# Optimization experiments

Hardware: AMD Instinct MI355X
Metric: run time of the kernel (lower is better)

The kernel has to match this reference:

```python
import jax, jax.numpy as jnp
import numpy as np

N, C, R, T, H, W = 2, 256, 8, 4, 32, 32
CK = C // R  # key channels = 32


def setup_inputs() -> dict:
    key = jax.random.key(0)
    ks = jax.random.split(key, 10)
    s = 0.05  # small init so dual softmax is not saturated
    return {
        "x1": jax.random.normal(ks[0], (N, C, T, H, W), jnp.float32),
        "x2": jax.random.normal(ks[1], (N, C, T, H, W), jnp.float32),
        "Wk1": jax.random.normal(ks[2], (CK, C), jnp.float32) * s,
        "bk1": jax.random.normal(ks[3], (CK,), jnp.float32) * s,
        "Wk2": jax.random.normal(ks[4], (CK, C), jnp.float32) * s,
        "bk2": jax.random.normal(ks[5], (CK,), jnp.float32) * s,
        "Wv1": jax.random.normal(ks[6], (C, C), jnp.float32) * s,
        "bv1": jax.random.normal(ks[7], (C,), jnp.float32) * s,
        "Wv2": jax.random.normal(ks[8], (C, C), jnp.float32) * s,
        "bv2": jax.random.normal(ks[9], (C,), jnp.float32) * s,
    }


def reference(x1, x2, Wk1, bk1, Wk2, bk2, Wv1, bv1, Wv2, bv2):
    n, c, t, h, w = x1.shape
    L = t * h * w
    x1f = x1.reshape(n, c, L)  # [n, C, L]
    x2f = x2.reshape(n, c, L)
    # 1x1x1 Conv3d == per-position channel mixing
    k1 = jnp.einsum('kc,ncl->nkl', Wk1, x1f) + bk1[None, :, None]  # [n, CK, L]
    k2 = jnp.einsum('kc,ncl->nkl', Wk2, x2f) + bk2[None, :, None]
    v1 = jnp.einsum('dc,ncl->ndl', Wv1, x1f) + bv1[None, :, None]  # [n, C, L]
    v2 = jnp.einsum('dc,ncl->ndl', Wv2, x2f) + bv2[None, :, None]
    # cor[n, l, m] = sum_k k1[n,k,l] * k2[n,k,m]
    cor = jnp.einsum('nkl,nkm->nlm', k1, k2)  # [n, L, L]
    attn1 = jax.nn.softmax(cor, axis=2)  # rows normalized
    attn2 = jax.nn.softmax(cor, axis=1)  # cols normalized
    r1 = jnp.einsum('ncl,nlm->ncm', v1, attn1).reshape(n, c, t, h, w)
    r2 = jnp.einsum('ncm,nlm->ncl', v2, attn2).reshape(n, c, t, h, w)
    return (x1 + r1, x2 + r2)
```

## Files before the change

### kernel.cpp

```cpp
#include <hip/hip_runtime.h>
#include <hip/hip_bf16.h>

#define N_  2
#define C_  256
#define CK_ 32
#define L_  4096

typedef __attribute__((ext_vector_type(8))) short short8;
typedef __attribute__((ext_vector_type(4))) float f32x4;
typedef __attribute__((ext_vector_type(2))) unsigned int uint2v;
typedef unsigned short ushort;

__device__ __forceinline__ ushort f2bf(float f){
  unsigned u = __float_as_uint(f);
  u += 0x7fffu + ((u >> 16) & 1u);
  return (ushort)(u >> 16);
}

__device__ __forceinline__ f32x4 mfma16(short8 a, short8 b, f32x4 c){
  return __builtin_amdgcn_mfma_f32_16x16x32_bf16(a, b, c, 0, 0, 0);
}

__global__ __launch_bounds__(256) void convert_xw_kernel(
    const float* __restrict__ x1, const float* __restrict__ x2,
    ushort* __restrict__ xT1, ushort* __restrict__ xT2,
    const float* __restrict__ Wk1, const float* __restrict__ Wk2,
    const float* __restrict__ Wv1, const float* __restrict__ Wv2,
    ushort* __restrict__ o1, ushort* __restrict__ o2,
    ushort* __restrict__ o3, ushort* __restrict__ o4){
  int b = blockIdx.x, t = threadIdx.x;
  if (b >= 512){
    int idx = (b - 512) * 256 + t;
    const int KS = CK_ * C_;
    const int VS = C_ * C_;
    if (idx < KS)                 o1[idx] = f2bf(Wk1[idx]);
    else if (idx < 2*KS)          o2[idx - KS] = f2bf(Wk2[idx - KS]);
    else if (idx < 2*KS + VS)     o3[idx - 2*KS] = f2bf(Wv1[idx - 2*KS]);
    else if (idx < 2*KS + 2*VS)   o4[idx - 2*KS - VS] = f2bf(Wv2[idx - 2*KS - VS]);
    return;
  }
  __shared__ float tt[32][264];
  int z = b & 3; int n = z & 1;
  const float* x = (z >> 1) ? x2 : x1;
  ushort* xT = (z >> 1) ? xT2 : xT1;
  int tile = b >> 2;
  int l0 = (tile & 15) * 256, c0 = (tile >> 4) * 32;
  int w = t >> 6, lam = t & 63;
  const float* xs = x + (size_t)n * C_ * L_;
  ushort* xd = xT + (size_t)n * L_ * C_;
#pragma unroll
  for (int k = 0; k < 8; ++k){
    int cr = w * 8 + k;
    float4 f = *(const float4*)(xs + (size_t)(c0 + cr) * L_ + l0 + lam * 4);
    *(float4*)&tt[cr][lam * 4] = f;
  }
  __syncthreads();
  int g = t & 3, lr = t >> 2;
#pragma unroll
  for (int k = 0; k < 4; ++k){
    int l = k * 64 + lr;
    union { __hip_bfloat162 h[4]; short8 v; } pk;
#pragma unroll
    for (int j = 0; j < 4; ++j)
      pk.h[j] = __float22bfloat162_rn(
          make_float2(tt[g*8 + 2*j][l], tt[g*8 + 2*j + 1][l]));
    *(short8*)(xd + (size_t)(l0 + l) * C_ + c0 + g * 8) = pk.v;
  }
}

#define VP_OFF(nn, cc, pp) \
  ((((size_t)(nn)*128 + ((pp)>>5))*16 + ((cc)>>4))*512 + \
   (((pp)&31)>>3)*128 + ((cc)&15)*8 + ((pp)&7))

__global__ __launch_bounds__(256) void proj_kernel(
    const ushort* __restrict__ xT1, const ushort* __restrict__ xT2,
    const ushort* __restrict__ Wk1b, const ushort* __restrict__ Wk2b,
    const ushort* __restrict__ Wv1b, const ushort* __restrict__ Wv2b,
    const float* __restrict__ bk1, const float* __restrict__ bk2,
    const float* __restrict__ bv1, const float* __restrict__ bv2,
    ushort* __restrict__ k1t, ushort* __restrict__ k2t,
    ushort* __restrict__ v1,  ushort* __restrict__ v2){
  int y = blockIdx.y, n = blockIdx.z;
  int t = threadIdx.x, w = t >> 6, lane = t & 63, quad = lane >> 4, low = lane & 15;
  const ushort* X; const ushort* W; const float* bias; ushort* outp; int jt; bool isK;
  if (y < 8)       { X = xT1; W = Wv1b; bias = bv1; outp = v1;  jt = y;     isK = false; }
  else if (y < 16) { X = xT2; W = Wv2b; bias = bv2; outp = v2;  jt = y - 8; isK = false; }
  else if (y == 16){ X = xT1; W = Wk1b; bias = bk1; outp = k1t; jt = 0;     isK = true; }
  else             { X = xT2; W = Wk2b; bias = bk2; outp = k2t; jt = 0;     isK = true; }
  int j0 = jt * 32;
  int l0 = blockIdx.x * 128 + w * 32;
  const ushort* Xn = X + (size_t)n * L_ * C_;
  f32x4 acc[2][2] = {};
#pragma unroll
  for (int kc = 0; kc < 8; ++kc){
    short8 a[2], b[2];
#pragma unroll
    for (int js = 0; js < 2; ++js)
      a[js] = *(const short8*)(W + (size_t)(j0 + js*16 + low)*C_ + kc*32 + quad*8);
#pragma unroll
    for (int ls = 0; ls < 2; ++ls)
      b[ls] = *(const short8*)(Xn + (size_t)(l0 + ls*16 + low)*C_ + kc*32 + quad*8);
#pragma unroll
    for (int js = 0; js < 2; ++js)
#pragma unroll
      for (int ls = 0; ls < 2; ++ls)
        acc[js][ls] = mfma16(a[js], b[ls], acc[js][ls]);
  }
#pragma unroll
  for (int js = 0; js < 2; ++js){
    f32x4 bb = *(const f32x4*)(bias + j0 + js*16 + quad*4);
#pragma unroll
    for (int ls = 0; ls < 2; ++ls){
      int l = l0 + ls*16 + low;
      if (!isK){
#pragma unroll
        for (int r = 0; r < 4; ++r){
          int c = j0 + js*16 + quad*4 + r;
          outp[VP_OFF(n, c, l)] = f2bf(acc[js][ls][r] + bb[r]);
        }
      } else {
        union { ushort u[4]; uint2v v; } pk;
#pragma unroll
        for (int r = 0; r < 4; ++r) pk.u[r] = f2bf(acc[js][ls][r] + bb[r]);
        *(uint2v*)(outp + ((size_t)n*L_ + l)*CK_ + j0 + js*16 + quad*4) = pk.v;
      }
    }
  }
}

__global__ __launch_bounds__(256) void stats_kernel(
    const ushort* __restrict__ k1t, const ushort* __restrict__ k2t,
    float* __restrict__ S1part, float* __restrict__ S2part){
  int n = blockIdx.z;
  int m0 = blockIdx.x * 128, l0 = blockIdx.y * 128;
  int t = threadIdx.x, w = t >> 6, lane = t & 63, quad = lane >> 4, low = lane & 15;
  __shared__ float rowsum[128];
  __shared__ float colsum[4][128];
  const ushort* ka = k1t + (size_t)n * L_ * CK_;
  const ushort* kb = k2t + (size_t)n * L_ * CK_;
  short8 a[2], b[8];
#pragma unroll
  for (int lt = 0; lt < 2; ++lt)
    a[lt] = *(const short8*)(ka + (size_t)(l0 + w*32 + lt*16 + low)*CK_ + quad*8);
#pragma unroll
  for (int mt = 0; mt < 8; ++mt)
    b[mt] = *(const short8*)(kb + (size_t)(m0 + mt*16 + low)*CK_ + quad*8);
  float rp[2][4] = {}; float cp[8] = {};
  const f32x4 zero = {0.f, 0.f, 0.f, 0.f};
#pragma unroll
  for (int lt = 0; lt < 2; ++lt)
#pragma unroll
    for (int mt = 0; mt < 8; ++mt){
      f32x4 e = mfma16(a[lt], b[mt], zero);
#pragma unroll
      for (int r = 0; r < 4; ++r){
        float v = __builtin_amdgcn_exp2f(e[r] * 1.44269504088896f);
        rp[lt][r] += v;
        cp[mt] += v;
      }
    }
#pragma unroll
  for (int lt = 0; lt < 2; ++lt)
#pragma unroll
    for (int r = 0; r < 4; ++r){
      float v = rp[lt][r];
      v += __shfl_xor(v, 1); v += __shfl_xor(v, 2);
      v += __shfl_xor(v, 4); v += __shfl_xor(v, 8);
      if (low == 0) rowsum[w*32 + lt*16 + quad*4 + r] = v;
    }
#pragma unroll
  for (int mt = 0; mt < 8; ++mt){
    float v = cp[mt];
    v += __shfl_xor(v, 16); v += __shfl_xor(v, 32);
    if (quad == 0) colsum[w][mt*16 + low] = v;
  }
  __syncthreads();
  if (t < 128)
    S1part[((size_t)n*32 + blockIdx.x)*L_ + l0 + t] = rowsum[t];
  else {
    int m = t - 128;
    S2part[((size_t)n*32 + blockIdx.y)*L_ + m0 + m] =
        colsum[0][m] + colsum[1][m] + colsum[2][m] + colsum[3][m];
  }
}

__global__ __launch_bounds__(256) void reduce_inv_kernel(
    const float* __restrict__ S1part, const float* __restrict__ S2part,
    float* __restrict__ invS1, float* __restrict__ invS2){
  int idx = blockIdx.x * 256 + threadIdx.x;
  int which = idx >> 13;
  int r = idx & 8191;
  int n = r >> 12, l = r & 4095;
  const float* P = which ? S2part : S1part;
  float s = 0.f;
#pragma unroll
  for (int j = 0; j < 32; ++j) s += P[((size_t)n*32 + j)*L_ + l];
  (which ? invS2 : invS1)[(size_t)n*L_ + l] = -__builtin_amdgcn_logf(s);
}

#define LOG2E_ 1.44269504088896f

__global__ __launch_bounds__(256, 2) void cross_attn_r_kernel(
    const ushort* __restrict__ k1t, const ushort* __restrict__ k2t,
    const ushort* __restrict__ v1,  const ushort* __restrict__ v2,
    const float* __restrict__ invS1, const float* __restrict__ invS2,
    const float* __restrict__ x1, const float* __restrict__ x2,
    float* __restrict__ out){
  int bid = blockIdx.x;
  int slice = bid & 7;
  int qb = bid >> 3;
  int n = slice & 1;
  int which = (slice >> 1) & 1;
  int chalf = slice >> 2;
  const ushort* kA = which ? k2t : k1t;
  const ushort* kB = which ? k1t : k2t;
  const ushort* V  = which ? v2  : v1;
  const float* iS  = which ? invS2 : invS1;
  const float* X   = which ? x2 : x1;
  float* O = out + (size_t)which * N_ * C_ * L_;
  int q0 = qb * 64, c0 = chalf * 128;
  int t = threadIdx.x, w = t >> 6, lane = t & 63, quad = lane >> 4, low = lane & 15;
  __shared__ __align__(16) float red[4][16][68];
  const ushort* kAn = kA + (size_t)n * L_ * CK_;
  const ushort* kBn = kB + (size_t)n * L_ * CK_;
  const float*  iSn = iS + (size_t)n * L_;

  const ushort* kA_base = kAn + (size_t)((low >> 2) * 8 + (low & 3)) * CK_ + quad * 8;
  const float*  sv_base = iSn + quad * 8;
  const ushort* Vp_lane = V + ((size_t)n * 128 * 16 + chalf * 8) * 512 + (size_t)lane * 8;

  short8 be[4];
#pragma unroll
  for (int qs = 0; qs < 4; ++qs)
    be[qs] = *(const short8*)(kBn + (size_t)(q0 + qs*16 + low) * CK_ + quad * 8);

  f32x4 acc[8][4] = {};
  const f32x4 zero = {0.f, 0.f, 0.f, 0.f};

  int pfirst = w * 32;
  short8 a0 = *(const short8*)(kA_base + (size_t)pfirst * CK_);
  short8 a1 = *(const short8*)(kA_base + (size_t)(pfirst + 4) * CK_);
  f32x4 sv0 = *(const f32x4*)(sv_base + pfirst);
  f32x4 sv1 = *(const f32x4*)(sv_base + pfirst + 4);

  short8 vv[8];
  {
    const ushort* vt0 = Vp_lane + (size_t)w * 16 * 512;
#pragma unroll
    for (int ct = 0; ct < 8; ++ct)
      vv[ct] = *(const short8*)(vt0 + ct * 512);
  }

#define EPH(PB, QS) do{                                                        \
    f32x4 e0 = mfma16(a0, be[QS], zero);                                       \
    f32x4 e1 = mfma16(a1, be[QS], zero);                                       \
    float p0 = __builtin_amdgcn_exp2f(__fmaf_rn(e0[0], LOG2E_, sv0[0]));       \
    float p1 = __builtin_amdgcn_exp2f(__fmaf_rn(e0[1], LOG2E_, sv0[1]));       \
    float p2 = __builtin_amdgcn_exp2f(__fmaf_rn(e0[2], LOG2E_, sv0[2]));       \
    float p3 = __builtin_amdgcn_exp2f(__fmaf_rn(e0[3], LOG2E_, sv0[3]));       \
    float p4 = __builtin_amdgcn_exp2f(__fmaf_rn(e1[0], LOG2E_, sv1[0]));       \
    float p5 = __builtin_amdgcn_exp2f(__fmaf_rn(e1[1], LOG2E_, sv1[1]));       \
    float p6 = __builtin_amdgcn_exp2f(__fmaf_rn(e1[2], LOG2E_, sv1[2]));       \
    float p7 = __builtin_amdgcn_exp2f(__fmaf_rn(e1[3], LOG2E_, sv1[3]));       \
    union { __hip_bfloat162 h[4]; short8 v; } pk;                              \
    pk.h[0] = __float22bfloat162_rn(make_float2(p0, p1));                      \
    pk.h[1] = __float22bfloat162_rn(make_float2(p2, p3));                      \
    pk.h[2] = __float22bfloat162_rn(make_float2(p4, p5));                      \
    pk.h[3] = __float22bfloat162_rn(make_float2(p6, p7));                      \
    PB = pk.v;                                                                 \
  }while(0)

  for (int kk = 0; kk < L_ / 256; ++kk){
#pragma unroll
    for (int half = 0; half < 2; ++half){
      int it = 2*kk + half;
      int itn = (it + 1) & 31;
      const ushort* vt_next = Vp_lane + (size_t)(itn*4 + w) * 16 * 512;
      int pn = itn * 128 + w * 32;
      short8 pb0, pb1;
      EPH(pb0, 0);
      EPH(pb1, 1);
      __builtin_amdgcn_s_setprio(1);
#pragma unroll
      for (int ct = 0; ct < 8; ++ct){
        acc[ct][0] = mfma16(vv[ct], pb0, acc[ct][0]);
        acc[ct][1] = mfma16(vv[ct], pb1, acc[ct][1]);
      }
      __builtin_amdgcn_s_setprio(0);
      EPH(pb0, 2);
      EPH(pb1, 3);
      a0 = *(const short8*)(kA_base + (size_t)pn * CK_);
      a1 = *(const short8*)(kA_base + (size_t)(pn + 4) * CK_);
      sv0 = *(const f32x4*)(sv_base + pn);
      sv1 = *(const f32x4*)(sv_base + pn + 4);
      __builtin_amdgcn_s_setprio(1);
#pragma unroll
      for (int ct = 0; ct < 8; ++ct){
        acc[ct][2] = mfma16(vv[ct], pb0, acc[ct][2]);
        acc[ct][3] = mfma16(vv[ct], pb1, acc[ct][3]);
        vv[ct] = *(const short8*)(vt_next + ct * 512);
      }
      __builtin_amdgcn_s_setprio(0);
    }
  }
#undef EPH

  int cl = t >> 4, qg = (t & 15) * 4;
#pragma unroll
  for (int ct = 0; ct < 8; ++ct){
#pragma unroll
    for (int qs = 0; qs < 4; ++qs)
#pragma unroll
      for (int r = 0; r < 4; ++r)
        red[w][quad*4 + r][qs*16 + low] = acc[ct][qs][r];
    __syncthreads();
    f32x4 s0 = *(const f32x4*)&red[0][cl][qg];
    f32x4 s1 = *(const f32x4*)&red[1][cl][qg];
    f32x4 s2 = *(const f32x4*)&red[2][cl][qg];
    f32x4 s3 = *(const f32x4*)&red[3][cl][qg];
    f32x4 s = (s0 + s1) + (s2 + s3);
    size_t idx = ((size_t)n * C_ + c0 + ct*16 + cl) * L_ + q0 + qg;
    const float4 xv = *(const float4*)(X + idx);
    float4 o = make_float4(xv.x + s[0], xv.y + s[1], xv.z + s[2], xv.w + s[3]);
    *(float4*)(O + idx) = o;
    __syncthreads();
  }
}

extern "C" void kernel_launch(void* const* d_in, const int* in_sizes, int n_in,
                              void* d_out, int out_size, void* d_ws, size_t ws_size,
                              hipStream_t stream) {
  const float* x1  = (const float*)d_in[0];
  const float* x2  = (const float*)d_in[1];
  const float* Wk1 = (const float*)d_in[2];
  const float* bk1 = (const float*)d_in[3];
  const float* Wk2 = (const float*)d_in[4];
  const float* bk2 = (const float*)d_in[5];
  const float* Wv1 = (const float*)d_in[6];
  const float* bv1 = (const float*)d_in[7];
  const float* Wv2 = (const float*)d_in[8];
  const float* bv2 = (const float*)d_in[9];

  char* ws = (char*)d_ws;
  size_t off = 0;
  auto carve = [&](size_t bytes) -> void* {
    void* p = ws + off; off += (bytes + 255) & ~(size_t)255; return p;
  };
  ushort* xT1   = (ushort*)carve((size_t)N_*L_*C_*2);
  ushort* xT2   = (ushort*)carve((size_t)N_*L_*C_*2);
  ushort* Wk1b  = (ushort*)carve((size_t)CK_*C_*2);
  ushort* Wk2b  = (ushort*)carve((size_t)CK_*C_*2);
  ushort* Wv1b  = (ushort*)carve((size_t)C_*C_*2);
  ushort* Wv2b  = (ushort*)carve((size_t)C_*C_*2);
  ushort* k1t   = (ushort*)carve((size_t)N_*L_*CK_*2);
  ushort* k2t   = (ushort*)carve((size_t)N_*L_*CK_*2);
  ushort* v1    = (ushort*)carve((size_t)N_*C_*L_*2);
  ushort* v2    = (ushort*)carve((size_t)N_*C_*L_*2);
  float*  S1p   = (float*)carve((size_t)N_*32*L_*4);
  float*  S2p   = (float*)carve((size_t)N_*32*L_*4);
  float*  invS1 = (float*)carve((size_t)N_*L_*4);
  float*  invS2 = (float*)carve((size_t)N_*L_*4);

  convert_xw_kernel<<<dim3(512 + (2*CK_*C_ + 2*C_*C_) / 256), 256, 0, stream>>>(
      x1, x2, xT1, xT2, Wk1, Wk2, Wv1, Wv2, Wk1b, Wk2b, Wv1b, Wv2b);
  proj_kernel<<<dim3(L_/128, 18, N_), 256, 0, stream>>>(
      xT1, xT2, Wk1b, Wk2b, Wv1b, Wv2b, bk1, bk2, bv1, bv2, k1t, k2t, v1, v2);
  stats_kernel<<<dim3(L_/128, L_/128, N_), 256, 0, stream>>>(k1t, k2t, S1p, S2p);
  reduce_inv_kernel<<<dim3(2*N_*L_/256), 256, 0, stream>>>(S1p, S2p, invS1, invS2);
  cross_attn_r_kernel<<<dim3(2 * N_ * (C_/128) * (L_/64), 1, 1), 256, 0, stream>>>(
      k1t, k2t, v1, v2, invS1, invS2, x1, x2, (float*)d_out);
}
```

Baseline: 165.6 us.

## Stage X tile in LDS and reuse it across output channel tiles in projection

The projection kernel now loads a 64-position by 256-channel X tile into shared memory once per block, then loops over 4 or 5 output-channel tiles (V tiles plus the K tile) reusing it. Before, each of the 18 y-blocks reread X from global memory. The grid is flattened to 512 blocks encoding batch, side, channel half and L tile. This cuts redundant X traffic but adds LDS use, a serialized loop over j-tiles per block, and per-iteration global weight loads.

```diff
diff --git a/kernel.cpp b/kernel.cpp
--- a/kernel.cpp
+++ b/kernel.cpp
@@ -80,49 +80,57 @@
     const float* __restrict__ bv1, const float* __restrict__ bv2,
     ushort* __restrict__ k1t, ushort* __restrict__ k2t,
     ushort* __restrict__ v1,  ushort* __restrict__ v2){
-  int y = blockIdx.y, n = blockIdx.z;
+  int bid = blockIdx.x;
+  int n = bid & 1, side = (bid >> 1) & 1, jh = (bid >> 2) & 1, ltile = bid >> 3;
+  const ushort* X  = side ? xT2 : xT1;
+  const ushort* Wv = side ? Wv2b : Wv1b;
+  const ushort* Wk = side ? Wk2b : Wk1b;
+  const float*  bv = side ? bv2 : bv1;
+  const float*  bk = side ? bk2 : bk1;
+  ushort* vout = side ? v2 : v1;
+  ushort* kout = side ? k2t : k1t;
+  int l0 = ltile * 64;
   int t = threadIdx.x, w = t >> 6, lane = t & 63, quad = lane >> 4, low = lane & 15;
-  const ushort* X; const ushort* W; const float* bias; ushort* outp; int jt; bool isK;
-  if (y < 8)       { X = xT1; W = Wv1b; bias = bv1; outp = v1;  jt = y;     isK = false; }
-  else if (y < 16) { X = xT2; W = Wv2b; bias = bv2; outp = v2;  jt = y - 8; isK = false; }
-  else if (y == 16){ X = xT1; W = Wk1b; bias = bk1; outp = k1t; jt = 0;     isK = true; }
-  else             { X = xT2; W = Wk2b; bias = bk2; outp = k2t; jt = 0;     isK = true; }
-  int j0 = jt * 32;
-  int l0 = blockIdx.x * 128 + w * 32;
-  const ushort* Xn = X + (size_t)n * L_ * C_;
-  f32x4 acc[2][2] = {};
-#pragma unroll
-  for (int kc = 0; kc < 8; ++kc){
-    short8 a[2], b[2];
-#pragma unroll
-    for (int js = 0; js < 2; ++js)
-      a[js] = *(const short8*)(W + (size_t)(j0 + js*16 + low)*C_ + kc*32 + quad*8);
-#pragma unroll
-    for (int ls = 0; ls < 2; ++ls)
-      b[ls] = *(const short8*)(Xn + (size_t)(l0 + ls*16 + low)*C_ + kc*32 + quad*8);
-#pragma unroll
-    for (int js = 0; js < 2; ++js)
-#pragma unroll
-      for (int ls = 0; ls < 2; ++ls)
-        acc[js][ls] = mfma16(a[js], b[ls], acc[js][ls]);
-  }
-#pragma unroll
-  for (int js = 0; js < 2; ++js){
-    f32x4 bb = *(const f32x4*)(bias + j0 + js*16 + quad*4);
-#pragma unroll
-    for (int ls = 0; ls < 2; ++ls){
-      int l = l0 + ls*16 + low;
+  __shared__ ushort xs[64][264];
+  const ushort* Xn = X + ((size_t)n * L_ + l0) * C_;
+#pragma unroll
+  for (int i = 0; i < 8; ++i){
+    int flat = i * 2048 + t * 8;
+    *(short8*)&xs[flat >> 8][flat & 255] = *(const short8*)(Xn + flat);
+  }
+  __syncthreads();
+  int lw = w * 16;
+  int l = l0 + lw + low;
+  int njt = jh ? 5 : 4;
+  for (int u = 0; u < njt; ++u){
+    int jt = jh ? (4 + u) : u;
+    bool isK = (jt == 8);
+    const ushort* W   = isK ? Wk : Wv + (size_t)jt * 32 * C_;
+    const float* bias = isK ? bk : bv + jt * 32;
+    f32x4 acc0 = {}, acc1 = {};
+#pragma unroll
+    for (int kc = 0; kc < 8; ++kc){
+      short8 b  = *(const short8*)&xs[lw + low][kc*32 + quad*8];
+      short8 a0 = *(const short8*)(W + (size_t)low * C_ + kc*32 + quad*8);
+      short8 a1 = *(const short8*)(W + (size_t)(16 + low) * C_ + kc*32 + quad*8);
+      acc0 = mfma16(a0, b, acc0);
+      acc1 = mfma16(a1, b, acc1);
+    }
+#pragma unroll
+    for (int js = 0; js < 2; ++js){
+      f32x4 acc = js ? acc1 : acc0;
+      f32x4 bb = *(const f32x4*)(bias + js*16 + quad*4);
       if (!isK){
 #pragma unroll
         for (int r = 0; r < 4; ++r){
-          int c = j0 + js*16 + quad*4 + r;
-          outp[VP_OFF(n, c, l)] = f2bf(acc[js][ls][r] + bb[r]);
+          int c = jt*32 + js*16 + quad*4 + r;
+          vout[VP_OFF(n, c, l)] = f2bf(acc[r] + bb[r]);
         }
       } else {
-        union { ushort u[4]; uint2v v; } pk;
-#pragma unroll
-        for (int r = 0; r < 4; ++r) pk.u[r] = f2bf(acc[js][ls][r] + bb[r]);
-        *(uint2v*)(outp + ((size_t)n*L_ + l)*CK_ + j0 + js*16 + quad*4) = pk.v;
+        union { ushort u4[4]; uint2v vv_; } pk;
+#pragma unroll
+        for (int r = 0; r < 4; ++r) pk.u4[r] = f2bf(acc[r] + bb[r]);
+        *(uint2v*)(kout + ((size_t)n*L_ + l)*CK_ + js*16 + quad*4) = pk.vv_;
       }
     }
   }
@@ -363,7 +371,7 @@
 
   convert_xw_kernel<<<dim3(512 + (2*CK_*C_ + 2*C_*C_) / 256), 256, 0, stream>>>(
       x1, x2, xT1, xT2, Wk1, Wk2, Wv1, Wv2, Wk1b, Wk2b, Wv1b, Wv2b);
-  proj_kernel<<<dim3(L_/128, 18, N_), 256, 0, stream>>>(
+  proj_kernel<<<dim3(512), 256, 0, stream>>>(
       xT1, xT2, Wk1b, Wk2b, Wv1b, Wv2b, bk1, bk2, bv1, bv2, k1t, k2t, v1, v2);
   stats_kernel<<<dim3(L_/128, L_/128, N_), 256, 0, stream>>>(k1t, k2t, S1p, S2p);
   reduce_inv_kernel<<<dim3(2*N_*L_/256), 256, 0, stream>>>(S1p, S2p, invS1, invS2);
```

Result: slower. 169.4 us (+2.3%).
